# Kernel tuning notes

Measured on AMD Instinct MI355X. Metric: run time of the kernel, lower is better.

Reference implementation:

```python
import jax, jax.numpy as jnp
import numpy as np

B, N_PER, E_PER = 128, 512, 8192          # graphs, nodes/graph, edges/graph
NUM_FEAT, NUM_REL, NUM_BASES = 4, 5, 2
LATENT = [32, 32, 32, 32]
D = 128                                    # sum(LATENT)
MAXN = 50                                  # self.max_neighbor
MAX_WALKS = 21
NUM_CLASSES = 5


def setup_inputs() -> dict:
    key = jax.random.key(0)
    ks = jax.random.split(key, 16)
    N, E = B * N_PER, B * E_PER
    # one-hot node-label features; node 0 of each graph = target user ([1,0,0,0]),
    # node 1 = target item ([0,1,0,0]), rest labels in {2,3}
    labels = jax.random.randint(ks[0], (B, N_PER), 2, NUM_FEAT)
    labels = labels.at[:, 0].set(0).at[:, 1].set(1)
    x = jax.nn.one_hot(labels.reshape(-1), NUM_FEAT, dtype=jnp.float32)
    offs = (jnp.arange(B, dtype=jnp.int32) * N_PER)[:, None]
    src = (jax.random.randint(ks[1], (B, E_PER), 0, N_PER).astype(jnp.int32) + offs).reshape(-1)
    dst = (jax.random.randint(ks[2], (B, E_PER), 0, N_PER).astype(jnp.int32) + offs).reshape(-1)
    edge_index = jnp.stack([src, dst])                       # [2, E] graph-local blocks
    edge_type = jax.random.randint(ks[3], (E,), 0, NUM_REL).astype(jnp.int32)
    batch = jnp.repeat(jnp.arange(B, dtype=jnp.int32), N_PER)
    inp = dict(x=x, edge_index=edge_index, edge_type=edge_type, batch=batch)
    dims = [NUM_FEAT] + LATENT
    ki = 4
    for l in range(4):
        fin, fout = dims[l], dims[l + 1]
        s = 1.0 / np.sqrt(fin)
        inp[f"basis{l}"] = (jax.random.normal(ks[ki], (NUM_BASES, fin, fout)) * s).astype(jnp.float32)
        inp[f"comp{l}"] = (jax.random.normal(ks[ki + 1], (NUM_REL, NUM_BASES)) * 0.5).astype(jnp.float32)
        inp[f"root{l}"] = (jax.random.normal(ks[ki + 2], (fin, fout)) * s).astype(jnp.float32)
        inp[f"cbias{l}"] = jnp.zeros((fout,), jnp.float32)
        ki += 3
    k2 = jax.random.split(jax.random.key(1), 4)
    inp["walk_w"] = (jax.random.normal(k2[0], (MAXN, D)) / np.sqrt(D)).astype(jnp.float32)
    inp["walk_b"] = jnp.zeros((MAXN,), jnp.float32)
    inp["lin1_w"] = (jax.random.normal(k2[1], (128, D)) / np.sqrt(D)).astype(jnp.float32)
    inp["lin1_b"] = jnp.zeros((128,), jnp.float32)
    inp["lin2_w"] = (jax.random.normal(k2[2], (NUM_CLASSES, 128)) / np.sqrt(128.0)).astype(jnp.float32)
    inp["lin2_b"] = jnp.zeros((NUM_CLASSES,), jnp.float32)
    return inp


def _rgcn(h, src, dst, etype, basis, comp, root, bias, n):
    # RGCNConv with basis decomposition: W_r = sum_b comp[r,b] * basis[b]; mean aggregation.
    hs = h[src]                                   # [E, fin]
    ce = comp[etype]                              # [E, num_bases]
    msg = ce[:, 0:1] * (hs @ basis[0])
    for b in range(1, NUM_BASES):
        msg = msg + ce[:, b:b + 1] * (hs @ basis[b])
    agg = jax.ops.segment_sum(msg, dst, num_segments=n)
    deg = jax.ops.segment_sum(jnp.ones(src.shape, msg.dtype), dst, num_segments=n)
    return agg / jnp.maximum(deg, 1.0)[:, None] + h @ root + bias


def _neighbor_table(src, dst, n):
    # per-node sorted out-neighbor lists, padded to MAXN with sentinel n
    E = src.shape[0]
    order = jnp.lexsort((dst, src))               # sort by src, then dst (== torch.sort of neighbors)
    s, d = src[order], dst[order]
    deg = jax.ops.segment_sum(jnp.ones((E,), jnp.int32), src, num_segments=n)
    offs = jnp.cumsum(deg) - deg
    rank = jnp.arange(E, dtype=jnp.int32) - offs[s]
    col = jnp.where(rank < MAXN, rank, MAXN)      # overflow -> dummy column
    table = jnp.full((n, MAXN + 1), n, jnp.int32).at[s, col].set(d)
    return table[:, :MAXN], deg


def _walk(xg, nbr, deg, start, end, w, b):
    # naive_reasoning_walking for one graph: xg [n,D], nbr [n,MAXN] local (pad=n), deg [n]
    n = xg.shape[0]
    trav0 = jnp.zeros((n,), bool).at[start].set(True)

    def step(state, _):
        node, acc, trav, done = state
        nb = jnp.clip(nbr[node], 0, n - 1)        # pads clipped; masked out below
        cnt = deg[node]
        no_nbr = cnt == 0
        logits = w @ acc + b                      # naive_walking_lin1(accumulated)
        valid = (jnp.arange(MAXN) < cnt) & ~trav[nb]
        sel = nb[jnp.argmax(jnp.where(valid, logits, -jnp.inf))]
        acc_new = acc + jnp.where(no_nbr, xg[end], xg[sel])
        upd = ~done
        move = upd & ~no_nbr
        acc = jnp.where(upd, acc_new, acc)
        trav = jnp.where(move, trav.at[sel].set(True), trav)
        done = done | (upd & (no_nbr | (sel == end)))
        node = jnp.where(move, sel, node)
        return (node, acc, trav, done), None

    (_, acc, trav, _), _ = jax.lax.scan(
        step, (start, xg[start], trav0, jnp.array(False)), None, length=MAX_WALKS)
    return acc / trav.sum().astype(acc.dtype)


def _forward(x, edge_index, edge_type, convs, walk_w, walk_b, lin1_w, lin1_b, lin2_w, lin2_b):
    N = x.shape[0]
    src, dst = edge_index[0], edge_index[1]
    h, states = x, []
    for basis, comp, root, bias in convs:
        h = jnp.tanh(_rgcn(h, src, dst, edge_type, basis, comp, root, bias, N))
        states.append(h)
    cs = jnp.concatenate(states, axis=1)          # [N, 128]
    table, deg = _neighbor_table(src, dst, N)
    # graphs are equal-sized (N_PER nodes each) -> per-graph local view
    tab = table.reshape(B, N_PER, MAXN)
    goff = (jnp.arange(B, dtype=jnp.int32) * N_PER)[:, None, None]
    tab_l = jnp.where(tab == N, N_PER, tab - goff)
    deg_l = deg.reshape(B, N_PER)
    xg = cs.reshape(B, N_PER, -1)
    start_l = jnp.argmax(x[:, 0].reshape(B, N_PER), axis=1)   # target user per graph
    end_l = jnp.argmax(x[:, 1].reshape(B, N_PER), axis=1)     # target item per graph
    pooled = jax.vmap(_walk, in_axes=(0, 0, 0, 0, 0, None, None))(
        xg, tab_l, deg_l, start_l, end_l, walk_w, walk_b)      # [B, 128]
    hid = jax.nn.relu(pooled @ lin1_w.T + lin1_b)              # dropout off (eval)
    logits = hid @ lin2_w.T + lin2_b
    return jax.nn.log_softmax(logits, axis=-1)


def reference(x, edge_index, edge_type, batch,
              basis0, comp0, root0, cbias0, basis1, comp1, root1, cbias1,
              basis2, comp2, root2, cbias2, basis3, comp3, root3, cbias3,
              walk_w, walk_b, lin1_w, lin1_b, lin2_w, lin2_b):
    # batch is implied by the fixed graph size; kept for interface fidelity
    convs = [(basis0, comp0, root0, cbias0), (basis1, comp1, root1, cbias1),
             (basis2, comp2, root2, cbias2), (basis3, comp3, root3, cbias3)]
    return _forward(x, edge_index, edge_type, convs,
                    walk_w, walk_b, lin1_w, lin1_b, lin2_w, lin2_b)
```

## Files before the change

kernel.cpp:

```cpp
#include <hip/hip_runtime.h>
#include <math.h>

#define NGRAPH 128
#define NPER   512
#define EPER   8192
#define NFEAT  4
#define NREL   5
#define DD     128
#define MAXNB  50
#define MAXW   21
#define NCLS   5

typedef unsigned short ushortT;
typedef unsigned char ucharT;

#define NTA 1024

__device__ __forceinline__ void scanExcl(const int* cnt, int* offs, int* tA,
                                         int* tB, int tid) {
  if (tid < NPER) tA[tid] = cnt[tid];
  __syncthreads();
  int* a = tA; int* b = tB;
  for (int d = 1; d < NPER; d <<= 1) {
    if (tid < NPER) {
      int v = a[tid];
      if (tid >= d) v += a[tid - d];
      b[tid] = v;
    }
    __syncthreads();
    int* t = a; a = b; b = t;
  }
  if (tid < NPER) offs[tid] = a[tid] - cnt[tid];
  __syncthreads();
}

__global__ __launch_bounds__(NTA, 1)
void build_csr2(const int* __restrict__ esrc, const int* __restrict__ edst,
                const int* __restrict__ etype, const float* __restrict__ x,
                ushortT* __restrict__ gBin, ushortT* __restrict__ gOut,
                int* __restrict__ pIn, int* __restrict__ pOut,
                int* __restrict__ gSE) {
  __shared__ int keyS[EPER];
  __shared__ int auxS[EPER];
  __shared__ ushortT nodS[EPER];
  __shared__ ucharT etyS[EPER];
  __shared__ int cnt[NPER], offs[NPER], fill[NPER];
  __shared__ int se[2];
  const int bid = blockIdx.x, tid = threadIdx.x;
  const int half = bid >> 7;
  const int g = bid & 127;
  const int nbase = g * NPER, ebase = g * EPER;

  if (tid < NPER) { cnt[tid] = 0; fill[tid] = 0; }
  if (tid < 2) se[tid] = NPER;
  __syncthreads();

  if (half == 0) {
    for (int e = tid; e < EPER; e += NTA) {
      auxS[e] = esrc[ebase + e] - nbase;
      etyS[e] = (ucharT)etype[ebase + e];
      int d = edst[ebase + e] - nbase;
      atomicAdd(&cnt[d], 1);
    }
    __syncthreads();
    scanExcl(cnt, offs, keyS, keyS + NPER, tid);
    for (int e = tid; e < EPER; e += NTA) {
      int d = edst[ebase + e] - nbase;
      int pos = offs[d] + atomicAdd(&fill[d], 1);
      keyS[pos] = (d << 13) | e;
    }
    __syncthreads();
    for (int p = tid; p < EPER; p += NTA) {
      const int k = keyS[p];
      const int n = k >> 13;
      const int o = offs[n], c = cnt[n];
      int r = 0;
      for (int i = 0; i < c; ++i) r += (keyS[o + i] < k);
      const int e = k & (EPER - 1);
      gBin[(size_t)g * EPER + o + r] = (ushortT)((auxS[e] << 3) | (int)etyS[e]);
    }
    if (tid < NPER) pIn[nbase + tid] = (offs[tid] << 14) | cnt[tid];
  } else {
    for (int e = tid; e < EPER; e += NTA) {
      int s = esrc[ebase + e] - nbase;
      auxS[e] = s;
      atomicAdd(&cnt[s], 1);
    }
    if (tid < NPER) {
      if (x[(size_t)(nbase + tid) * NFEAT + 0] > 0.5f) atomicMin(&se[0], tid);
      if (x[(size_t)(nbase + tid) * NFEAT + 1] > 0.5f) atomicMin(&se[1], tid);
    }
    __syncthreads();
    scanExcl(cnt, offs, keyS, keyS + NPER, tid);
    for (int e = tid; e < EPER; e += NTA) {
      int s = auxS[e];
      int d = edst[ebase + e] - nbase;
      int pos = offs[s] + atomicAdd(&fill[s], 1);
      keyS[pos] = (d << 13) | e;
      nodS[pos] = (ushortT)s;
    }
    __syncthreads();
    for (int p = tid; p < EPER; p += NTA) {
      const int k = keyS[p];
      const int n = (int)nodS[p];
      const int o = offs[n], c = cnt[n];
      int r = 0;
      for (int i = 0; i < c; ++i) r += (keyS[o + i] < k);
      gOut[(size_t)g * EPER + o + r] = (ushortT)(k >> 13);
    }
    if (tid < NPER) pOut[nbase + tid] = (offs[tid] << 14) | cnt[tid];
    if (tid < 2) gSE[g * 2 + tid] = (se[tid] >= NPER) ? 0 : se[tid];
  }
}

template <int FIN>
__global__ __launch_bounds__(512, 1)
void rgcn_layer2p(const float* __restrict__ x, float* __restrict__ cs,
                  const ushortT* __restrict__ gBin, const int* __restrict__ pIn,
                  const float* __restrict__ bas, const float* __restrict__ cmp,
                  const float* __restrict__ rt, const float* __restrict__ bi,
                  int l) {
  constexpr int NK4 = (3 * FIN) / 4;
  constexpr int LPN = FIN / 4;
  __shared__ float A_s[NK4 * 256 * 4];
  __shared__ float Bt_s[NK4 * 32 * 4];
  __shared__ float compS[NREL * 2];
  const int bid = blockIdx.x, tid = threadIdx.x;
  const int g = bid >> 1, half = bid & 1;
  const int nbase = g * NPER;
  const int nb2 = nbase + half * 256;

  for (int idx = tid; idx < NK4 * 128; idx += 512) {
    const int k4 = idx >> 7, rem = idx & 127;
    const int o = rem >> 2, c = rem & 3;
    const int k = k4 * 4 + c;
    float v;
    if (k < 2 * FIN) v = bas[k * 32 + o];
    else v = rt[(k - 2 * FIN) * 32 + o];
    Bt_s[(k4 * 32 + o) * 4 + c] = v;
  }
  if (tid < NREL * 2) compS[tid] = cmp[tid];
  for (int idx = tid; idx < 256 * LPN; idx += 512) {
    const int n = idx / LPN, kq = idx % LPN;
    float4 hv;
    if constexpr (FIN == 4)
      hv = *(const float4*)(x + (size_t)(nb2 + n) * NFEAT);
    else
      hv = *(const float4*)(cs + (size_t)(nb2 + n) * DD + (l - 1) * 32 + kq * 4);
    *(float4*)&A_s[((2 * LPN + kq) * 256 + n) * 4] = hv;
  }
  __syncthreads();

  for (int t = tid; t < 256 * LPN; t += 512) {
    const int n = t / LPN, q = t % LPN;
    const int pk = pIn[nb2 + n];
    const int off = pk >> 14, c = pk & 16383;
    const float inv = 1.0f / (float)(c > 1 ? c : 1);
    float4 s0 = make_float4(0.f, 0.f, 0.f, 0.f);
    float4 s1 = make_float4(0.f, 0.f, 0.f, 0.f);
    const ushortT* el = gBin + (size_t)g * EPER + off;
    const float* hb;
    if constexpr (FIN == 4) hb = x + (size_t)nbase * NFEAT;
    else hb = cs + (size_t)nbase * DD + (l - 1) * 32 + q * 4;
    constexpr int STRIDE = (FIN == 4) ? NFEAT : DD;
    if (c > 0) {
      int pe = (int)el[0];
      float4 hv = *(const float4*)(hb + (size_t)(pe >> 3) * STRIDE);
      for (int i = 0; i + 1 < c; ++i) {
        const int pe_n = (int)el[i + 1];
        const float4 hv_n = *(const float4*)(hb + (size_t)(pe_n >> 3) * STRIDE);
        const float c0 = compS[(pe & 7) * 2], c1 = compS[(pe & 7) * 2 + 1];
        s0.x = fmaf(c0, hv.x, s0.x); s0.y = fmaf(c0, hv.y, s0.y);
        s0.z = fmaf(c0, hv.z, s0.z); s0.w = fmaf(c0, hv.w, s0.w);
        s1.x = fmaf(c1, hv.x, s1.x); s1.y = fmaf(c1, hv.y, s1.y);
        s1.z = fmaf(c1, hv.z, s1.z); s1.w = fmaf(c1, hv.w, s1.w);
        pe = pe_n; hv = hv_n;
      }
      const float c0 = compS[(pe & 7) * 2], c1 = compS[(pe & 7) * 2 + 1];
      s0.x = fmaf(c0, hv.x, s0.x); s0.y = fmaf(c0, hv.y, s0.y);
      s0.z = fmaf(c0, hv.z, s0.z); s0.w = fmaf(c0, hv.w, s0.w);
      s1.x = fmaf(c1, hv.x, s1.x); s1.y = fmaf(c1, hv.y, s1.y);
      s1.z = fmaf(c1, hv.z, s1.z); s1.w = fmaf(c1, hv.w, s1.w);
    }
    s0.x *= inv; s0.y *= inv; s0.z *= inv; s0.w *= inv;
    s1.x *= inv; s1.y *= inv; s1.z *= inv; s1.w *= inv;
    *(float4*)&A_s[(q * 256 + n) * 4] = s0;
    *(float4*)&A_s[((LPN + q) * 256 + n) * 4] = s1;
  }
  __syncthreads();

  const int ot = (tid >> 4) & 3;
  const int nt = (tid & 15) | ((tid >> 6) << 4);
  const int n0 = 2 * nt, o0 = 8 * ot;
  float acc[2][8];
#pragma unroll
  for (int i = 0; i < 2; ++i)
#pragma unroll
    for (int j = 0; j < 8; ++j) acc[i][j] = 0.f;
  for (int k4 = 0; k4 < NK4; ++k4) {
    const float4 a0 = *(const float4*)&A_s[(k4 * 256 + n0) * 4];
    const float4 a1 = *(const float4*)&A_s[(k4 * 256 + n0 + 1) * 4];
#pragma unroll
    for (int j = 0; j < 8; ++j) {
      const float4 b = *(const float4*)&Bt_s[(k4 * 32 + o0 + j) * 4];
      acc[0][j] = fmaf(a0.x, b.x, acc[0][j]);
      acc[0][j] = fmaf(a0.y, b.y, acc[0][j]);
      acc[0][j] = fmaf(a0.z, b.z, acc[0][j]);
      acc[0][j] = fmaf(a0.w, b.w, acc[0][j]);
      acc[1][j] = fmaf(a1.x, b.x, acc[1][j]);
      acc[1][j] = fmaf(a1.y, b.y, acc[1][j]);
      acc[1][j] = fmaf(a1.z, b.z, acc[1][j]);
      acc[1][j] = fmaf(a1.w, b.w, acc[1][j]);
    }
  }
#pragma unroll
  for (int i = 0; i < 2; ++i) {
    float4 w0, w1;
    w0.x = tanhf(acc[i][0] + bi[o0 + 0]); w0.y = tanhf(acc[i][1] + bi[o0 + 1]);
    w0.z = tanhf(acc[i][2] + bi[o0 + 2]); w0.w = tanhf(acc[i][3] + bi[o0 + 3]);
    w1.x = tanhf(acc[i][4] + bi[o0 + 4]); w1.y = tanhf(acc[i][5] + bi[o0 + 5]);
    w1.z = tanhf(acc[i][6] + bi[o0 + 6]); w1.w = tanhf(acc[i][7] + bi[o0 + 7]);
    float* dst = cs + (size_t)(nb2 + n0 + i) * DD + l * 32 + o0;
    *(float4*)dst = w0;
    *(float4*)(dst + 4) = w1;
  }
}

__global__ __launch_bounds__(256, 1)
void walk_head4(const float* __restrict__ cs, const ushortT* __restrict__ gOut,
                const int* __restrict__ pOut, const int* __restrict__ gSE,
                const float* __restrict__ walk_w, const float* __restrict__ walk_b,
                const float* __restrict__ lin1_w, const float* __restrict__ lin1_b,
                const float* __restrict__ lin2_w, const float* __restrict__ lin2_b,
                float* __restrict__ out) {
  __shared__ float wT2[64 * 136];
  __shared__ float rowS[DD];
  __shared__ ushortT gOutS[EPER];
  __shared__ int pOutS[NPER];
  __shared__ int travS[NPER];
  __shared__ int listS[MAXW + 2];
  __shared__ int scal[4];
  __shared__ float pooledS[DD], hidS[DD], logitsS[8];
  const int g = blockIdx.x, tid = threadIdx.x;
  const int nbase = g * NPER;

  for (int i = tid; i < 64 * 128; i += 256) {
    const int j = i >> 7, k = i & 127;
    wT2[j * 136 + k] = (j < MAXNB) ? walk_w[j * DD + k] : 0.f;
  }
  {
    const unsigned int* g32 = (const unsigned int*)(gOut + (size_t)g * EPER);
    unsigned int* s32 = (unsigned int*)gOutS;
    for (int i = tid; i < EPER / 2; i += 256) s32[i] = g32[i];
    for (int i = tid; i < NPER; i += 256) {
      pOutS[i] = pOut[nbase + i];
      travS[i] = 0;
    }
  }
  const int startN = gSE[2 * g];
  const int endN = gSE[2 * g + 1];
  if (tid < 64)
    ((float2*)rowS)[tid] = ((const float2*)(cs + (size_t)(nbase + startN) * DD))[tid];
  if (tid == 0) { travS[startN] = 1; listS[0] = startN; }
  __syncthreads();

  if (tid < 64) {
    const int j = tid;
    const float* wrow = wT2 + j * 136;
    float l = (j < MAXNB) ? walk_b[j] : 0.f;
#pragma unroll
    for (int k4 = 0; k4 < 32; ++k4) {
      const float4 r = *(const float4*)&rowS[k4 * 4];
      const float4 w = *(const float4*)&wrow[k4 * 4];
      l = fmaf(w.w, r.w, fmaf(w.z, r.z, fmaf(w.y, r.y, fmaf(w.x, r.x, l))));
    }
    int node = startN, visited = 1, nrows = 1;
    for (int step = 0; step < MAXW; ++step) {
      const int pk = pOutS[node];
      const int off = pk >> 14, c = pk & 16383;
      const int jm = (c < MAXNB) ? c : MAXNB;
      float myval = -INFINITY;
      if (j < jm) {
        const int nb = (int)gOutS[off + j];
        if (!travS[nb]) myval = l;
      }
      int myidx = j;
#pragma unroll
      for (int o = 1; o < 64; o <<= 1) {
        const float ov = __shfl_xor(myval, o, 64);
        const int oi = __shfl_xor(myidx, o, 64);
        if (ov > myval || (ov == myval && oi < myidx)) { myval = ov; myidx = oi; }
      }
      const bool no_nbr = (c == 0);
      const int sel = no_nbr ? 0 : (int)gOutS[off + myidx];
      const int tgt = no_nbr ? endN : sel;
      if (j == 0) listS[nrows] = tgt;
      nrows++;
      const float2 rv = ((const float2*)(cs + (size_t)(nbase + tgt) * DD))[j];
      ((float2*)rowS)[j] = rv;
#pragma unroll
      for (int k4 = 0; k4 < 32; ++k4) {
        const float4 r = *(const float4*)&rowS[k4 * 4];
        const float4 w = *(const float4*)&wrow[k4 * 4];
        l = fmaf(w.w, r.w, fmaf(w.z, r.z, fmaf(w.y, r.y, fmaf(w.x, r.x, l))));
      }
      if (!no_nbr) {
        if (j == 0) travS[sel] = 1;
        visited++;
        node = sel;
      }
      if (no_nbr || sel == endN) break;
    }
    if (j == 0) { scal[0] = nrows; scal[1] = visited; }
  }
  __syncthreads();

  const int nrows = scal[0];
  if (tid < DD) {
    float acc = cs[(size_t)(nbase + listS[0]) * DD + tid];
    for (int t = 1; t < nrows; ++t)
      acc += cs[(size_t)(nbase + listS[t]) * DD + tid];
    pooledS[tid] = acc / (float)scal[1];
  }
  __syncthreads();
  if (tid < DD) {
    const float4* w4 = (const float4*)(lin1_w + (size_t)tid * DD);
    float s = lin1_b[tid];
#pragma unroll 8
    for (int k4 = 0; k4 < DD / 4; ++k4) {
      const float4 wv = w4[k4];
      s += wv.x * pooledS[k4 * 4 + 0] + wv.y * pooledS[k4 * 4 + 1]
         + wv.z * pooledS[k4 * 4 + 2] + wv.w * pooledS[k4 * 4 + 3];
    }
    hidS[tid] = fmaxf(s, 0.f);
  }
  __syncthreads();
  if (tid < NCLS) {
    const float4* w4 = (const float4*)(lin2_w + (size_t)tid * DD);
    float s = lin2_b[tid];
#pragma unroll 8
    for (int k4 = 0; k4 < DD / 4; ++k4) {
      const float4 wv = w4[k4];
      s += wv.x * hidS[k4 * 4 + 0] + wv.y * hidS[k4 * 4 + 1]
         + wv.z * hidS[k4 * 4 + 2] + wv.w * hidS[k4 * 4 + 3];
    }
    logitsS[tid] = s;
  }
  __syncthreads();
  if (tid < NCLS) {
    float m = logitsS[0];
    for (int c = 1; c < NCLS; ++c) m = fmaxf(m, logitsS[c]);
    float sum = 0.f;
    for (int c = 0; c < NCLS; ++c) sum += expf(logitsS[c] - m);
    const float lse = m + logf(sum);
    out[g * NCLS + tid] = logitsS[tid] - lse;
  }
}

extern "C" void kernel_launch(void* const* d_in, const int* in_sizes, int n_in,
                              void* d_out, int out_size, void* d_ws, size_t ws_size,
                              hipStream_t stream) {
  const float* x = (const float*)d_in[0];
  const int* ei = (const int*)d_in[1];
  const int E = in_sizes[1] / 2;
  const int* esrc = ei;
  const int* edst = ei + E;
  const int* et = (const int*)d_in[2];

  char* ws = (char*)d_ws;
  float* cs = (float*)ws;
  size_t off = (size_t)NGRAPH * NPER * DD * sizeof(float);
  ushortT* gBin = (ushortT*)(ws + off); off += (size_t)NGRAPH * EPER * sizeof(ushortT);
  ushortT* gOut = (ushortT*)(ws + off); off += (size_t)NGRAPH * EPER * sizeof(ushortT);
  int* pIn = (int*)(ws + off); off += (size_t)NGRAPH * NPER * sizeof(int);
  int* pOut = (int*)(ws + off); off += (size_t)NGRAPH * NPER * sizeof(int);
  int* gSE = (int*)(ws + off); off += (size_t)NGRAPH * 2 * sizeof(int);

  build_csr2<<<dim3(2 * NGRAPH), dim3(NTA), 0, stream>>>(esrc, edst, et, x, gBin,
                                                         gOut, pIn, pOut, gSE);
  rgcn_layer2p<NFEAT><<<dim3(2 * NGRAPH), dim3(512), 0, stream>>>(
      x, cs, gBin, pIn, (const float*)d_in[4], (const float*)d_in[5],
      (const float*)d_in[6], (const float*)d_in[7], 0);
  rgcn_layer2p<32><<<dim3(2 * NGRAPH), dim3(512), 0, stream>>>(
      x, cs, gBin, pIn, (const float*)d_in[8], (const float*)d_in[9],
      (const float*)d_in[10], (const float*)d_in[11], 1);
  rgcn_layer2p<32><<<dim3(2 * NGRAPH), dim3(512), 0, stream>>>(
      x, cs, gBin, pIn, (const float*)d_in[12], (const float*)d_in[13],
      (const float*)d_in[14], (const float*)d_in[15], 2);
  rgcn_layer2p<32><<<dim3(2 * NGRAPH), dim3(512), 0, stream>>>(
      x, cs, gBin, pIn, (const float*)d_in[16], (const float*)d_in[17],
      (const float*)d_in[18], (const float*)d_in[19], 3);
  walk_head4<<<dim3(NGRAPH), dim3(256), 0, stream>>>(
      cs, gOut, pOut, gSE, (const float*)d_in[20], (const float*)d_in[21],
      (const float*)d_in[22], (const float*)d_in[23], (const float*)d_in[24],
      (const float*)d_in[25], (float*)d_out);
}
```

Baseline: 170.1 us.

## Precompute walk projection for all nodes via GEMM, accumulate logits incrementally

Adds a parallel GEMM that projects every node's 128-dim embedding onto the 50 walk weights into a workspace buffer. A new walk head keeps a running logit vector by adding precomputed rows along the walk, replacing per-step matrix work in the serial walk loop. The RGCN block-to-graph mapping also changes so the two halves of a graph land in separate grid halves. The trade is an extra kernel launch and about 16 MB of extra global writes and reads, plus a dependence on workspace size; the old path remains as a fallback.

```diff
diff --git a/kernel.cpp b/kernel.cpp
--- a/kernel.cpp
+++ b/kernel.cpp
@@ -126,7 +126,7 @@
   __shared__ float Bt_s[NK4 * 32 * 4];
   __shared__ float compS[NREL * 2];
   const int bid = blockIdx.x, tid = threadIdx.x;
-  const int g = bid >> 1, half = bid & 1;
+  const int g = bid & 127, half = bid >> 7;
   const int nbase = g * NPER;
   const int nb2 = nbase + half * 256;
 
@@ -227,6 +227,175 @@
 }
 
 __global__ __launch_bounds__(256, 1)
+void p_gemm(const float* __restrict__ cs, const float* __restrict__ walk_w,
+            float* __restrict__ P) {
+  __shared__ float A_s[32 * 128 * 4];
+  __shared__ float BtS[32 * 64 * 4];
+  const int bid = blockIdx.x, tid = threadIdx.x;
+  const int g = bid & 127, quad = bid >> 7;
+  const int nb2 = g * NPER + quad * 128;
+
+  for (int idx = tid; idx < 64 * 32; idx += 256) {
+    const int j = idx >> 5, k4 = idx & 31;
+    float4 v = make_float4(0.f, 0.f, 0.f, 0.f);
+    if (j < MAXNB) v = *(const float4*)(walk_w + j * DD + k4 * 4);
+    *(float4*)&BtS[(k4 * 64 + j) * 4] = v;
+  }
+  for (int idx = tid; idx < 128 * 32; idx += 256) {
+    const int n = idx >> 5, k4 = idx & 31;
+    const float4 v = *(const float4*)(cs + (size_t)(nb2 + n) * DD + k4 * 4);
+    *(float4*)&A_s[(k4 * 128 + n) * 4] = v;
+  }
+  __syncthreads();
+
+  const int nt = tid & 31, jt = tid >> 5;
+  const int n0 = 4 * nt, j0 = 8 * jt;
+  float acc[4][8];
+#pragma unroll
+  for (int i = 0; i < 4; ++i)
+#pragma unroll
+    for (int j = 0; j < 8; ++j) acc[i][j] = 0.f;
+  for (int k4 = 0; k4 < 32; ++k4) {
+    const float4 a0 = *(const float4*)&A_s[(k4 * 128 + n0 + 0) * 4];
+    const float4 a1 = *(const float4*)&A_s[(k4 * 128 + n0 + 1) * 4];
+    const float4 a2 = *(const float4*)&A_s[(k4 * 128 + n0 + 2) * 4];
+    const float4 a3 = *(const float4*)&A_s[(k4 * 128 + n0 + 3) * 4];
+#pragma unroll
+    for (int j = 0; j < 8; ++j) {
+      const float4 b = *(const float4*)&BtS[(k4 * 64 + j0 + j) * 4];
+      acc[0][j] = fmaf(a0.x, b.x, acc[0][j]); acc[0][j] = fmaf(a0.y, b.y, acc[0][j]);
+      acc[0][j] = fmaf(a0.z, b.z, acc[0][j]); acc[0][j] = fmaf(a0.w, b.w, acc[0][j]);
+      acc[1][j] = fmaf(a1.x, b.x, acc[1][j]); acc[1][j] = fmaf(a1.y, b.y, acc[1][j]);
+      acc[1][j] = fmaf(a1.z, b.z, acc[1][j]); acc[1][j] = fmaf(a1.w, b.w, acc[1][j]);
+      acc[2][j] = fmaf(a2.x, b.x, acc[2][j]); acc[2][j] = fmaf(a2.y, b.y, acc[2][j]);
+      acc[2][j] = fmaf(a2.z, b.z, acc[2][j]); acc[2][j] = fmaf(a2.w, b.w, acc[2][j]);
+      acc[3][j] = fmaf(a3.x, b.x, acc[3][j]); acc[3][j] = fmaf(a3.y, b.y, acc[3][j]);
+      acc[3][j] = fmaf(a3.z, b.z, acc[3][j]); acc[3][j] = fmaf(a3.w, b.w, acc[3][j]);
+    }
+  }
+#pragma unroll
+  for (int i = 0; i < 4; ++i) {
+    float4 w0, w1;
+    w0.x = acc[i][0]; w0.y = acc[i][1]; w0.z = acc[i][2]; w0.w = acc[i][3];
+    w1.x = acc[i][4]; w1.y = acc[i][5]; w1.z = acc[i][6]; w1.w = acc[i][7];
+    float* dst = P + (size_t)(nb2 + n0 + i) * 64 + j0;
+    *(float4*)dst = w0;
+    *(float4*)(dst + 4) = w1;
+  }
+}
+
+__global__ __launch_bounds__(256, 1)
+void walk_head5(const float* __restrict__ cs, const float* __restrict__ P,
+                const ushortT* __restrict__ gOut, const int* __restrict__ pOut,
+                const int* __restrict__ gSE, const float* __restrict__ walk_b,
+                const float* __restrict__ lin1_w, const float* __restrict__ lin1_b,
+                const float* __restrict__ lin2_w, const float* __restrict__ lin2_b,
+                float* __restrict__ out) {
+  __shared__ ushortT gOutS[EPER];
+  __shared__ int pOutS[NPER];
+  __shared__ int travS[NPER];
+  __shared__ int listS[MAXW + 2];
+  __shared__ int scal[4];
+  __shared__ float pooledS[DD], hidS[DD], logitsS[8];
+  const int g = blockIdx.x, tid = threadIdx.x;
+  const int nbase = g * NPER;
+  const float* Pg = P + (size_t)nbase * 64;
+
+  {
+    const unsigned int* g32 = (const unsigned int*)(gOut + (size_t)g * EPER);
+    unsigned int* s32 = (unsigned int*)gOutS;
+    for (int i = tid; i < EPER / 2; i += 256) s32[i] = g32[i];
+    for (int i = tid; i < NPER; i += 256) {
+      pOutS[i] = pOut[nbase + i];
+      travS[i] = 0;
+    }
+  }
+  const int startN = gSE[2 * g];
+  const int endN = gSE[2 * g + 1];
+  if (tid == 0) { travS[startN] = 1; listS[0] = startN; }
+  __syncthreads();
+
+  if (tid < 64) {
+    const int j = tid;
+    float l = 0.f;
+    if (j < MAXNB) l = Pg[(size_t)startN * 64 + j] + walk_b[j];
+    int node = startN, visited = 1, nrows = 1;
+    for (int step = 0; step < MAXW; ++step) {
+      const int pk = pOutS[node];
+      const int off = pk >> 14, c = pk & 16383;
+      const int jm = (c < MAXNB) ? c : MAXNB;
+      float myval = -INFINITY;
+      if (j < jm) {
+        const int nb = (int)gOutS[off + j];
+        if (!travS[nb]) myval = l;
+      }
+      int myidx = j;
+#pragma unroll
+      for (int o = 1; o < 64; o <<= 1) {
+        const float ov = __shfl_xor(myval, o, 64);
+        const int oi = __shfl_xor(myidx, o, 64);
+        if (ov > myval || (ov == myval && oi < myidx)) { myval = ov; myidx = oi; }
+      }
+      const bool no_nbr = (c == 0);
+      const int sel = no_nbr ? 0 : (int)gOutS[off + myidx];
+      const int tgt = no_nbr ? endN : sel;
+      if (j == 0) listS[nrows] = tgt;
+      nrows++;
+      if (j < MAXNB) l += Pg[(size_t)tgt * 64 + j];
+      if (!no_nbr) {
+        if (j == 0) travS[sel] = 1;
+        visited++;
+        node = sel;
+      }
+      if (no_nbr || sel == endN) break;
+    }
+    if (j == 0) { scal[0] = nrows; scal[1] = visited; }
+  }
+  __syncthreads();
+
+  const int nrows = scal[0];
+  if (tid < DD) {
+    float acc = cs[(size_t)(nbase + listS[0]) * DD + tid];
+    for (int t = 1; t < nrows; ++t)
+      acc += cs[(size_t)(nbase + listS[t]) * DD + tid];
+    pooledS[tid] = acc / (float)scal[1];
+  }
+  __syncthreads();
+  if (tid < DD) {
+    const float4* w4 = (const float4*)(lin1_w + (size_t)tid * DD);
+    float s = lin1_b[tid];
+#pragma unroll 8
+    for (int k4 = 0; k4 < DD / 4; ++k4) {
+      const float4 wv = w4[k4];
+      s += wv.x * pooledS[k4 * 4 + 0] + wv.y * pooledS[k4 * 4 + 1]
+         + wv.z * pooledS[k4 * 4 + 2] + wv.w * pooledS[k4 * 4 + 3];
+    }
+    hidS[tid] = fmaxf(s, 0.f);
+  }
+  __syncthreads();
+  if (tid < NCLS) {
+    const float4* w4 = (const float4*)(lin2_w + (size_t)tid * DD);
+    float s = lin2_b[tid];
+#pragma unroll 8
+    for (int k4 = 0; k4 < DD / 4; ++k4) {
+      const float4 wv = w4[k4];
+      s += wv.x * hidS[k4 * 4 + 0] + wv.y * hidS[k4 * 4 + 1]
+         + wv.z * hidS[k4 * 4 + 2] + wv.w * hidS[k4 * 4 + 3];
+    }
+    logitsS[tid] = s;
+  }
+  __syncthreads();
+  if (tid < NCLS) {
+    float m = logitsS[0];
+    for (int c = 1; c < NCLS; ++c) m = fmaxf(m, logitsS[c]);
+    float sum = 0.f;
+    for (int c = 0; c < NCLS; ++c) sum += expf(logitsS[c] - m);
+    const float lse = m + logf(sum);
+    out[g * NCLS + tid] = logitsS[tid] - lse;
+  }
+}
+
+__global__ __launch_bounds__(256, 1)
 void walk_head4(const float* __restrict__ cs, const ushortT* __restrict__ gOut,
                 const int* __restrict__ pOut, const int* __restrict__ gSE,
                 const float* __restrict__ walk_w, const float* __restrict__ walk_b,
@@ -375,6 +544,10 @@
   int* pIn = (int*)(ws + off); off += (size_t)NGRAPH * NPER * sizeof(int);
   int* pOut = (int*)(ws + off); off += (size_t)NGRAPH * NPER * sizeof(int);
   int* gSE = (int*)(ws + off); off += (size_t)NGRAPH * 2 * sizeof(int);
+  off = (off + 255) & ~(size_t)255;
+  float* Pbuf = (float*)(ws + off);
+  const size_t pBytes = (size_t)NGRAPH * NPER * 64 * sizeof(float);
+  const bool haveP = (ws_size >= off + pBytes);
 
   build_csr2<<<dim3(2 * NGRAPH), dim3(NTA), 0, stream>>>(esrc, edst, et, x, gBin,
                                                          gOut, pIn, pOut, gSE);
@@ -390,8 +563,17 @@
   rgcn_layer2p<32><<<dim3(2 * NGRAPH), dim3(512), 0, stream>>>(
       x, cs, gBin, pIn, (const float*)d_in[16], (const float*)d_in[17],
       (const float*)d_in[18], (const float*)d_in[19], 3);
-  walk_head4<<<dim3(NGRAPH), dim3(256), 0, stream>>>(
-      cs, gOut, pOut, gSE, (const float*)d_in[20], (const float*)d_in[21],
-      (const float*)d_in[22], (const float*)d_in[23], (const float*)d_in[24],
-      (const float*)d_in[25], (float*)d_out);
-}
+  if (haveP) {
+    p_gemm<<<dim3(4 * NGRAPH), dim3(256), 0, stream>>>(
+        cs, (const float*)d_in[20], Pbuf);
+    walk_head5<<<dim3(NGRAPH), dim3(256), 0, stream>>>(
+        cs, Pbuf, gOut, pOut, gSE, (const float*)d_in[21],
+        (const float*)d_in[22], (const float*)d_in[23], (const float*)d_in[24],
+        (const float*)d_in[25], (float*)d_out);
+  } else {
+    walk_head4<<<dim3(NGRAPH), dim3(256), 0, stream>>>(
+        cs, gOut, pOut, gSE, (const float*)d_in[20], (const float*)d_in[21],
+        (const float*)d_in[22], (const float*)d_in[23], (const float*)d_in[24],
+        (const float*)d_in[25], (float*)d_out);
+  }
+}
```

Result: no change. 167.8 us, median of 2 (-1.4%).
